# Performance work log

Hardware: AMD Instinct MI355X
Metric: run time of the kernel (lower is better)

The kernel has to match this reference:

```python
import jax, jax.numpy as jnp
import numpy as np

L = 3
NUM_NODES = 4000
NUM_RELS = 200
V = 20
EMB = 128
HID = 128
OUT = 100
N = 50000
E = 800000
B = 32
DECAY = 0.03


def setup_inputs() -> dict:
    key = jax.random.key(0)
    ks = jax.random.split(key, 20)
    s = 0.05  # weight scale
    inp = {
        'node_emb': jax.random.normal(ks[0], (NUM_NODES, EMB), jnp.float32) * s,
        'rel_emb': jax.random.normal(ks[1], (NUM_RELS, EMB), jnp.float32) * s,
        'lin_w': jax.random.normal(ks[2], (HID, EMB), jnp.float32) * s,  # torch Linear weight [out,in]
        'lin_b': jnp.zeros((HID,), jnp.float32),
        'alpha_w': jax.random.normal(ks[3], (L, NUM_NODES, NUM_NODES), jnp.float32) * 0.01,
        'alpha_b': jnp.zeros((L, NUM_NODES), jnp.float32),
        'beta_w': jax.random.normal(ks[4], (L, NUM_NODES), jnp.float32) * 0.01,
        'beta_b': jnp.zeros((L,), jnp.float32),
        'wr_w': jax.random.normal(ks[5], (L, HID), jnp.float32) * s,
        'wr_b': jnp.zeros((L,), jnp.float32),
        'conv_w': jax.random.normal(ks[6], (L, HID, HID), jnp.float32) * s,
        'conv_b': jnp.zeros((L, HID), jnp.float32),
        'mlp_w': jax.random.normal(ks[7], (OUT, 2 * HID), jnp.float32) * s,
        'mlp_b': jnp.zeros((OUT,), jnp.float32),
        'visit_node': jax.random.uniform(ks[8], (B, V, NUM_NODES), jnp.float32),
        'ehr_nodes': jax.random.uniform(ks[9], (B, NUM_NODES), jnp.float32),
        'node_ids': jax.random.randint(ks[10], (N,), 0, NUM_NODES, jnp.int32),
        'rel_ids': jax.random.randint(ks[11], (E,), 0, NUM_RELS, jnp.int32),
        'edge_index': jax.random.randint(ks[12], (2, E), 0, N, jnp.int32),
        'batch': jnp.sort(jax.random.randint(ks[13], (N,), 0, B, jnp.int32)),
    }
    return inp


def reference(node_emb, rel_emb, lin_w, lin_b, alpha_w, alpha_b, beta_w, beta_b,
              wr_w, wr_b, conv_w, conv_b, mlp_w, mlp_b, visit_node, ehr_nodes,
              node_ids, rel_ids, edge_index, batch):
    # initial node / edge features
    x = node_emb[node_ids] @ lin_w.T + lin_b                # [N, HID]
    edge_attr = rel_emb[rel_ids] @ lin_w.T + lin_b          # [E, HID]

    # temporal decay per visit: lambda_j = exp(decay*(V - j)), shape [1, V, 1]
    j = jnp.arange(V, dtype=jnp.float32)
    lam = jnp.exp(DECAY * (V - j))[None, :, None]

    src = edge_index[0]
    dst = edge_index[1]
    xj_nid = node_ids[src]                                  # [E]
    xj_bat = batch[src]                                     # [E]

    for l in range(L):
        # alpha: softmax over the visit axis (dim=1)
        alpha = jax.nn.softmax(
            jnp.einsum('bvn,mn->bvm', visit_node, alpha_w[l]) + alpha_b[l], axis=1)
        beta = jnp.tanh(
            jnp.einsum('bvn,n->bv', visit_node, beta_w[l])[:, :, None] + beta_b[l]) * lam
        attn = jnp.sum(alpha * beta, axis=1)                # [B, NUM_NODES]
        e_attn = attn[xj_bat, xj_nid][:, None]              # [E, 1]

        # BiAttentionGNNConv message + add-aggregate
        w_rel = edge_attr @ wr_w[l][:, None] + wr_b[l]      # [E, 1]
        msg = jax.nn.relu(x[src] * e_attn + w_rel * edge_attr)
        agg = jax.ops.segment_sum(msg, dst, num_segments=N)
        out = agg + x                                       # eps = 0 -> (1+eps)=1
        x = out @ conv_w[l].T + conv_b[l]                   # conv.nn Linear
        x = jax.nn.relu(x)                                  # outer F.relu (dropout inactive in eval)

    # global mean pool over graphs
    cnt = jax.ops.segment_sum(jnp.ones((N,), x.dtype), batch, num_segments=B)
    x_graph = jax.ops.segment_sum(x, batch, num_segments=B) / jnp.maximum(cnt, 1.0)[:, None]

    # patient node embedding branch
    x_node = (ehr_nodes @ node_emb) / jnp.sum(ehr_nodes, axis=1, keepdims=True)
    x_node = x_node @ lin_w.T + lin_b                       # [B, HID]

    logits = jnp.concatenate([x_graph, x_node], axis=1) @ mlp_w.T + mlp_b
    return logits
```

## Files before the change

kernel.cpp:

```cpp
#include <hip/hip_runtime.h>
#include <hip/hip_bf16.h>
#include <stdint.h>

#define LL      3
#define NNODES  4000
#define NRELS   200
#define VV      20
#define EMB     128
#define HIDD    128
#define OUTD    100
#define WS_N    50000
#define WS_E    800000
#define BV      32
#define DECAYF  0.03f
#define AK      4032
#define ZSTRIDE ((long)LL*640*4000)
#define SCAN_NB 196
#define NPP     391
#define CVT_NB  (BV*VV + LL*NNODES)
#define CNT_NB  ((WS_E+255)/256)

typedef __bf16 bf16x8 __attribute__((ext_vector_type(8)));
typedef __bf16 bf16x4 __attribute__((ext_vector_type(4)));
typedef __bf16 bf16x2 __attribute__((ext_vector_type(2)));
typedef float  f32x4  __attribute__((ext_vector_type(4)));

__device__ __forceinline__ void glds16(const __bf16* g, __bf16* l) {
    __builtin_amdgcn_global_load_lds((const __attribute__((address_space(1))) void*)g,
                                     (__attribute__((address_space(3))) void*)l, 16, 0, 0);
}

__global__ __launch_bounds__(256) void k_cvt2(const float* __restrict__ visit,
                                              const float* __restrict__ alpha_w,
                                              const float* __restrict__ beta_w,
                                              const float* __restrict__ beta_b,
                                              __bf16* __restrict__ visit_bf,
                                              __bf16* __restrict__ alpha_bf,
                                              float* __restrict__ betab,
                                              const int* __restrict__ edst,
                                              int* __restrict__ deg) {
    long bid = blockIdx.x;
    int t = threadIdx.x;
    if (bid >= CVT_NB) {
        int e = (int)(bid - CVT_NB)*256 + t;
        if (e < WS_E) atomicAdd(&deg[edst[e]], 1);
        return;
    }
    const bool isv = bid < BV*VV;
    const float* ip; __bf16* op;
    if (isv) { ip = visit + bid*4000; op = visit_bf + bid*AK; }
    else     { long r = bid - BV*VV; ip = alpha_w + r*4000; op = alpha_bf + r*AK; }
    float p0 = 0.f, p1 = 0.f, p2 = 0.f;
    if (t < 250) {
        const float4* p4 = (const float4*)ip + t*4;
        float4 f0 = p4[0], f1 = p4[1], f2 = p4[2], f3 = p4[3];
        bf16x8 h0, h1;
        h0[0]=(__bf16)f0.x; h0[1]=(__bf16)f0.y; h0[2]=(__bf16)f0.z; h0[3]=(__bf16)f0.w;
        h0[4]=(__bf16)f1.x; h0[5]=(__bf16)f1.y; h0[6]=(__bf16)f1.z; h0[7]=(__bf16)f1.w;
        h1[0]=(__bf16)f2.x; h1[1]=(__bf16)f2.y; h1[2]=(__bf16)f2.z; h1[3]=(__bf16)f2.w;
        h1[4]=(__bf16)f3.x; h1[5]=(__bf16)f3.y; h1[6]=(__bf16)f3.z; h1[7]=(__bf16)f3.w;
        ((bf16x8*)op)[t*2]   = h0;
        ((bf16x8*)op)[t*2+1] = h1;
        if (isv) {
            #pragma unroll
            for (int l = 0; l < LL; l++) {
                const float4* bw = (const float4*)(beta_w + (long)l*4000) + t*4;
                float4 b0 = bw[0], b1 = bw[1], b2 = bw[2], b3 = bw[3];
                float s = f0.x*b0.x + f0.y*b0.y + f0.z*b0.z + f0.w*b0.w
                        + f1.x*b1.x + f1.y*b1.y + f1.z*b1.z + f1.w*b1.w
                        + f2.x*b2.x + f2.y*b2.y + f2.z*b2.z + f2.w*b2.w
                        + f3.x*b3.x + f3.y*b3.y + f3.z*b3.z + f3.w*b3.w;
                if (l == 0) p0 = s; else if (l == 1) p1 = s; else p2 = s;
            }
        }
    } else if (t < 254) {
        bf16x8 zz;
        #pragma unroll
        for (int j = 0; j < 8; j++) zz[j] = (__bf16)0.f;
        ((bf16x8*)op)[500 + (t - 250)] = zz;
    }
    if (isv) {
        __shared__ float r0[256], r1[256], r2[256];
        r0[t] = p0; r1[t] = p1; r2[t] = p2;
        __syncthreads();
        for (int o = 128; o > 0; o >>= 1) {
            if (t < o) { r0[t] += r0[t+o]; r1[t] += r1[t+o]; r2[t] += r2[t+o]; }
            __syncthreads();
        }
        if (t == 0) {
            int v = (int)(bid % VV);
            float lam = __expf(DECAYF * (float)(VV - v));
            betab[0*BV*VV + bid] = tanhf(r0[0] + beta_b[0]) * lam;
            betab[1*BV*VV + bid] = tanhf(r1[0] + beta_b[1]) * lam;
            betab[2*BV*VV + bid] = tanhf(r2[0] + beta_b[2]) * lam;
        }
    }
}

__global__ __launch_bounds__(256)
void gemm_alpha(const __bf16* __restrict__ visit_bf, const __bf16* __restrict__ alpha_bf,
                __bf16* __restrict__ zpart)
{
    __shared__ __bf16 Ah[128*64];
    __shared__ __bf16 Bh[128*64];

    const int id   = blockIdx.x;
    const int xcd  = id & 7;
    const int slot = id >> 3;
    const int mi   = slot % 5;
    const int gix  = slot / 5;
    const int g    = xcd * 48 + gix;
    const int ni   = g & 31;
    const int lkh  = g >> 5;
    const int l    = lkh >> 2;
    const int kh   = lkh & 3;

    const __bf16* Ag = visit_bf;
    const __bf16* Bg = alpha_bf + (long)l * NNODES * AK;
    __bf16*       Cg = zpart + (long)kh * ZSTRIDE + (long)l * 640 * 4000;
    const int m0 = mi * 128;
    const int n0 = ni * 128;
    const int k0 = kh * 1024;
    const int k1 = (kh == 3) ? AK : (k0 + 1024);

    const int tid = threadIdx.x;
    const int wv  = tid >> 6;
    const int ln  = tid & 63;
    const int srow = ln >> 3;
    const int gsl  = (ln & 7) ^ srow;

    const __bf16* aA = Ag + (long)(m0 + wv*8 + srow) * AK + gsl*8;
    const __bf16* bB[4];
    #pragma unroll
    for (int t = 0; t < 4; t++) {
        int br = n0 + wv*8 + srow + t*32;
        if (br > NNODES-1) br = NNODES-1;
        bB[t] = Bg + (long)br * AK + gsl*8;
    }

    const int wm = (wv & 1) * 64;
    const int wn = (wv >> 1) * 64;
    const int lr = ln & 15;
    const int kq = ln >> 4;
    const int sw0 = lr & 7;

    f32x4 acc[4][4];
    #pragma unroll
    for (int i = 0; i < 4; i++)
        #pragma unroll
        for (int j = 0; j < 4; j++)
            acc[i][j] = (f32x4){0.f, 0.f, 0.f, 0.f};

    for (int kb = k0; kb < k1; kb += 64) {
        #pragma unroll
        for (int t = 0; t < 4; t++) {
            glds16(aA + (long)t*32*AK + kb, &Ah[(t*4 + wv) * 512]);
            glds16(bB[t] + kb,              &Bh[(t*4 + wv) * 512]);
        }
        __syncthreads();
        #pragma unroll
        for (int ks = 0; ks < 2; ks++) {
            const int sg = ((ks*4 + kq) ^ sw0) * 8;
            bf16x8 af[4], bfr[4];
            #pragma unroll
            for (int i = 0; i < 4; i++) {
                af[i]  = *(const bf16x8*)&Ah[(wm + i*16 + lr)*64 + sg];
                bfr[i] = *(const bf16x8*)&Bh[(wn + i*16 + lr)*64 + sg];
            }
            #pragma unroll
            for (int i = 0; i < 4; i++)
                #pragma unroll
                for (int j = 0; j < 4; j++)
                    acc[i][j] = __builtin_amdgcn_mfma_f32_16x16x32_bf16(af[i], bfr[j], acc[i][j], 0, 0, 0);
        }
        __syncthreads();
    }

    #pragma unroll
    for (int i = 0; i < 4; i++) {
        const int row_b = m0 + wm + i*16 + kq*4;
        #pragma unroll
        for (int j = 0; j < 4; j++) {
            const int col = n0 + wn + j*16 + lr;
            if (col < NNODES) {
                #pragma unroll
                for (int r = 0; r < 4; r++)
                    Cg[(long)(row_b + r)*4000 + col] = (__bf16)acc[i][j][r];
            }
        }
    }
}

#define BM 128
#define BN 128
#define BKG 32
#define LSTR 40

template<int SPLIT>
__device__ __forceinline__ void stage_tile(const float* __restrict__ G, int rows, int Kdim,
                                           int r0, int kb, int k1, __bf16* Sh, __bf16* Sl, int tid)
{
    const int sr  = tid >> 1;
    const int skc = (tid & 1) * 16;
    const int gr  = r0 + sr;
    const int gk  = kb + skc;
    float va[16];
    if (gr < rows && gk + 16 <= k1) {
        const float4* p4 = (const float4*)(G + (long)gr * Kdim + gk);
        #pragma unroll
        for (int q = 0; q < 4; q++) {
            float4 f = p4[q];
            va[4*q+0] = f.x; va[4*q+1] = f.y; va[4*q+2] = f.z; va[4*q+3] = f.w;
        }
    } else {
        #pragma unroll
        for (int j = 0; j < 16; j++) {
            int kk = gk + j;
            va[j] = (gr < rows && kk < k1) ? G[(long)gr * Kdim + kk] : 0.0f;
        }
    }
    bf16x8 h[2], lo[2];
    #pragma unroll
    for (int half = 0; half < 2; half++) {
        #pragma unroll
        for (int j = 0; j < 8; j++) {
            float v = va[half*8 + j];
            __bf16 hi = (__bf16)v;
            h[half][j]  = hi;
            lo[half][j] = (__bf16)(v - (float)hi);
        }
    }
    *(bf16x8*)&Sh[sr*LSTR + skc]     = h[0];
    *(bf16x8*)&Sh[sr*LSTR + skc + 8] = h[1];
    if (SPLIT) {
        *(bf16x8*)&Sl[sr*LSTR + skc]     = lo[0];
        *(bf16x8*)&Sl[sr*LSTR + skc + 8] = lo[1];
    }
}

template<int SPLIT, int RELU, int BIAS, int WRITEB>
__global__ __launch_bounds__(256)
void gemm_bt(const float* __restrict__ Ag, const float* __restrict__ Bg,
             float* __restrict__ Cg, const float* __restrict__ bias,
             __bf16* __restrict__ Xb, int M, int N, int K)
{
    __shared__ __bf16 Ah[BM*LSTR];
    __shared__ __bf16 Bh[BN*LSTR];
    __shared__ __bf16 Alo[SPLIT ? BM*LSTR : 1];
    __shared__ __bf16 Blo[SPLIT ? BN*LSTR : 1];

    const int tid = threadIdx.x;
    const int m0 = blockIdx.x * BM;
    const int n0 = blockIdx.y * BN;

    const int wave = tid >> 6;
    const int lane = tid & 63;
    const int wm = (wave & 1) * 64;
    const int wn = (wave >> 1) * 64;
    const int lr = lane & 15;
    const int kq = lane >> 4;

    f32x4 acc[4][4];
    #pragma unroll
    for (int i = 0; i < 4; i++)
        #pragma unroll
        for (int j = 0; j < 4; j++)
            acc[i][j] = (f32x4){0.f, 0.f, 0.f, 0.f};

    for (int kb = 0; kb < K; kb += BKG) {
        stage_tile<SPLIT>(Ag, M, K, m0, kb, K, Ah, Alo, tid);
        stage_tile<SPLIT>(Bg, N, K, n0, kb, K, Bh, Blo, tid);
        __syncthreads();

        bf16x8 af[4], bfr[4];
        #pragma unroll
        for (int i = 0; i < 4; i++) {
            af[i]  = *(const bf16x8*)&Ah[(wm + i*16 + lr)*LSTR + kq*8];
            bfr[i] = *(const bf16x8*)&Bh[(wn + i*16 + lr)*LSTR + kq*8];
        }
        #pragma unroll
        for (int i = 0; i < 4; i++)
            #pragma unroll
            for (int j = 0; j < 4; j++)
                acc[i][j] = __builtin_amdgcn_mfma_f32_16x16x32_bf16(af[i], bfr[j], acc[i][j], 0, 0, 0);

        if (SPLIT) {
            bf16x8 al[4], bl[4];
            #pragma unroll
            for (int i = 0; i < 4; i++) {
                al[i] = *(const bf16x8*)&Alo[(wm + i*16 + lr)*LSTR + kq*8];
                bl[i] = *(const bf16x8*)&Blo[(wn + i*16 + lr)*LSTR + kq*8];
            }
            #pragma unroll
            for (int i = 0; i < 4; i++)
                #pragma unroll
                for (int j = 0; j < 4; j++) {
                    acc[i][j] = __builtin_amdgcn_mfma_f32_16x16x32_bf16(af[i], bl[j], acc[i][j], 0, 0, 0);
                    acc[i][j] = __builtin_amdgcn_mfma_f32_16x16x32_bf16(al[i], bfr[j], acc[i][j], 0, 0, 0);
                }
        }
        __syncthreads();
    }

    #pragma unroll
    for (int i = 0; i < 4; i++) {
        const int row_b = m0 + wm + i*16 + kq*4;
        #pragma unroll
        for (int j = 0; j < 4; j++) {
            const int col = n0 + wn + j*16 + lr;
            if (col < N) {
                #pragma unroll
                for (int r = 0; r < 4; r++) {
                    const int row = row_b + r;
                    if (row < M) {
                        float v = acc[i][j][r];
                        if (BIAS) v += bias[col];
                        if (RELU) v = fmaxf(v, 0.0f);
                        Cg[(long)row*N + col] = v;
                        if (WRITEB) Xb[(long)row*N + col] = (__bf16)v;
                    }
                }
            }
        }
    }
}

__global__ __launch_bounds__(256) void k_scan1(const int* __restrict__ deg, int* __restrict__ bsum) {
    __shared__ int red[256];
    int t = threadIdx.x;
    int i = blockIdx.x*256 + t;
    red[t] = (i < WS_N) ? deg[i] : 0;
    __syncthreads();
    for (int o = 128; o > 0; o >>= 1) {
        if (t < o) red[t] += red[t + o];
        __syncthreads();
    }
    if (t == 0) bsum[blockIdx.x] = red[0];
}

__global__ __launch_bounds__(256) void k_scan3(const int* __restrict__ deg, const int* __restrict__ bsum,
                                               int* __restrict__ offs, int* __restrict__ cursor) {
    __shared__ int sb[256];
    __shared__ int s[256];
    int t = threadIdx.x;
    int bv = (t < SCAN_NB) ? bsum[t] : 0;
    sb[t] = bv;
    __syncthreads();
    for (int o = 1; o < 256; o <<= 1) {
        int add = (t >= o) ? sb[t - o] : 0;
        __syncthreads();
        sb[t] += add;
        __syncthreads();
    }
    int base = (blockIdx.x == 0) ? 0 : sb[blockIdx.x - 1];

    int i = blockIdx.x*256 + t;
    int v = (i < WS_N) ? deg[i] : 0;
    s[t] = v;
    __syncthreads();
    for (int o = 1; o < 256; o <<= 1) {
        int add = (t >= o) ? s[t - o] : 0;
        __syncthreads();
        s[t] += add;
        __syncthreads();
    }
    if (i < WS_N) {
        int e = base + s[t] - v;
        offs[i] = e;
        cursor[i] = e;
    }
    if (blockIdx.x == 0 && t == 0) offs[WS_N] = WS_E;
}

__global__ void k_fill(const int* __restrict__ dst, const int* __restrict__ src,
                       const int* __restrict__ rel, int* __restrict__ cursor,
                       uint32_t* __restrict__ sr) {
    int e = blockIdx.x*256 + threadIdx.x;
    if (e < WS_E) {
        int d = dst[e];
        int p = atomicAdd(&cursor[d], 1);
        sr[p] = (uint32_t)src[e] | ((uint32_t)rel[e] << 16);
    }
}

__global__ __launch_bounds__(128) void k_relfused(const float* __restrict__ rel_emb,
                                                  const float* __restrict__ lin_w,
                                                  const float* __restrict__ lin_b,
                                                  const float* __restrict__ wr_w,
                                                  const float* __restrict__ wr_b,
                                                  __bf16* __restrict__ relmsg) {
    int r = blockIdx.x;
    int o = threadIdx.x;
    __shared__ float row[128];
    __shared__ float red[128];
    row[o] = rel_emb[(long)r*EMB + o];
    __syncthreads();
    float wv = lin_b[o];
    #pragma unroll 4
    for (int k = 0; k < EMB; k++) wv += row[k] * lin_w[(long)o*EMB + k];
    #pragma unroll
    for (int l = 0; l < LL; l++) {
        red[o] = wv * wr_w[l*HIDD + o];
        __syncthreads();
        for (int s2 = 64; s2 > 0; s2 >>= 1) {
            if (o < s2) red[o] += red[o + s2];
            __syncthreads();
        }
        float wrel = red[0] + wr_b[l];
        __syncthreads();
        relmsg[((long)l*NRELS + r)*HIDD + o] = (__bf16)(wrel * wv);
    }
}

__global__ void k_xinit(const float* __restrict__ Wnode, const int* __restrict__ nid,
                        const int* __restrict__ batch, const float* __restrict__ attn,
                        float* __restrict__ x, __bf16* __restrict__ xb, float* __restrict__ an) {
    int t = blockIdx.x*256 + threadIdx.x;
    if (t >= WS_N*32) return;
    int i = t >> 5;
    int d = t & 31;
    int n = nid[i];
    float4 v = ((const float4*)Wnode)[n*32 + d];
    ((float4*)x)[i*32 + d] = v;
    bf16x4 b;
    b[0] = (__bf16)v.x; b[1] = (__bf16)v.y; b[2] = (__bf16)v.z; b[3] = (__bf16)v.w;
    ((bf16x4*)xb)[i*32 + d] = b;
    if (d < LL) an[(long)d*WS_N + i] = attn[((long)d*BV + batch[i]) * NNODES + n];
}

__global__ __launch_bounds__(256) void k_attnpool(const __bf16* __restrict__ zpart,
                                                  const float* __restrict__ beta, float* __restrict__ attn) {
    int m = blockIdx.x*256 + threadIdx.x;
    int b = blockIdx.y;
    int l = blockIdx.z;
    if (m >= NNODES) return;
    const __bf16* zp = zpart + ((long)l*640 + b*VV) * 4000 + m;
    const float* bet = beta + (l*BV + b) * VV;
    float zv[VV];
    float mx = -1e30f;
    #pragma unroll
    for (int v = 0; v < VV; v++) {
        long o = (long)v * 4000;
        float s = (float)zp[o] + (float)zp[ZSTRIDE + o] + (float)zp[2*ZSTRIDE + o] + (float)zp[3*ZSTRIDE + o];
        zv[v] = s;
        mx = fmaxf(mx, s);
    }
    float s = 0.f, ws = 0.f;
    #pragma unroll
    for (int v = 0; v < VV; v++) {
        float e = __expf(zv[v] - mx);
        s += e;
        ws += e * bet[v];
    }
    attn[((long)l*BV + b) * NNODES + m] = ws / s;
}

__global__ __launch_bounds__(256) void k_agg(const float* __restrict__ x, const __bf16* __restrict__ xb,
                                             const float* __restrict__ an,
                                             const __bf16* __restrict__ relmsg_l, const int* __restrict__ offs,
                                             const uint32_t* __restrict__ sr,
                                             float* __restrict__ outb) {
    int node = blockIdx.x*4 + (threadIdx.x >> 6);
    int lane = threadIdx.x & 63;
    int eh = lane >> 4;
    int lh = lane & 15;
    int e0 = offs[node], e1 = offs[node + 1];
    const bf16x8* xb8 = (const bf16x8*)xb;
    const bf16x8* rm8 = (const bf16x8*)relmsg_l;
    float acc[8];
    #pragma unroll
    for (int d = 0; d < 8; d++) acc[d] = 0.f;
    int e = e0;
    for (; e + 8 <= e1; e += 8) {
        uint32_t p0 = sr[e + eh], p1 = sr[e + 4 + eh];
        int s0 = p0 & 0xFFFF, r0 = p0 >> 16;
        int s1 = p1 & 0xFFFF, r1 = p1 >> 16;
        float a0 = an[s0], a1 = an[s1];
        bf16x8 g0 = xb8[s0*16 + lh], g1 = xb8[s1*16 + lh];
        bf16x8 m0 = rm8[r0*16 + lh], m1 = rm8[r1*16 + lh];
        #pragma unroll
        for (int d = 0; d < 8; d++) {
            acc[d] += fmaxf((float)g0[d]*a0 + (float)m0[d], 0.f);
            acc[d] += fmaxf((float)g1[d]*a1 + (float)m1[d], 0.f);
        }
    }
    for (; e + 4 <= e1; e += 4) {
        uint32_t p = sr[e + eh];
        int s = p & 0xFFFF, r = p >> 16;
        float a = an[s];
        bf16x8 g = xb8[s*16 + lh];
        bf16x8 m = rm8[r*16 + lh];
        #pragma unroll
        for (int d = 0; d < 8; d++)
            acc[d] += fmaxf((float)g[d]*a + (float)m[d], 0.f);
    }
    if (e + eh < e1) {
        uint32_t p = sr[e + eh];
        int s = p & 0xFFFF, r = p >> 16;
        float a = an[s];
        bf16x8 g = xb8[s*16 + lh];
        bf16x8 m = rm8[r*16 + lh];
        #pragma unroll
        for (int d = 0; d < 8; d++)
            acc[d] += fmaxf((float)g[d]*a + (float)m[d], 0.f);
    }
    #pragma unroll
    for (int d = 0; d < 8; d++) {
        acc[d] += __shfl_xor(acc[d], 16);
        acc[d] += __shfl_xor(acc[d], 32);
    }
    if (eh == 0) {
        float4 x0 = ((const float4*)x)[node*32 + lh*2];
        float4 x1 = ((const float4*)x)[node*32 + lh*2 + 1];
        float4 o0, o1;
        o0.x = acc[0] + x0.x; o0.y = acc[1] + x0.y; o0.z = acc[2] + x0.z; o0.w = acc[3] + x0.w;
        o1.x = acc[4] + x1.x; o1.y = acc[5] + x1.y; o1.z = acc[6] + x1.z; o1.w = acc[7] + x1.w;
        ((float4*)outb)[node*32 + lh*2]     = o0;
        ((float4*)outb)[node*32 + lh*2 + 1] = o1;
    }
}

__global__ __launch_bounds__(256) void k_pool(const float* __restrict__ x,
                                              const int* __restrict__ batch,
                                              const float* __restrict__ ehr,
                                              const float* __restrict__ node_emb,
                                              float* __restrict__ xgsum,
                                              float* __restrict__ xnsum,
                                              float* __restrict__ esum) {
    if (blockIdx.x < NPP) {
        int r0 = blockIdx.x * 128;
        int d = threadIdx.x & 127;
        int rofs = threadIdx.x >> 7;
        int r1 = min(r0 + 128, WS_N);
        float acc = 0.f;
        int curb = -1;
        for (int i = r0 + rofs; i < r1; i += 2) {
            int b = batch[i];
            if (b != curb) {
                if (curb >= 0) atomicAdd(&xgsum[curb*HIDD + d], acc);
                acc = 0.f; curb = b;
            }
            acc += x[(long)i*HIDD + d];
        }
        if (curb >= 0) atomicAdd(&xgsum[curb*HIDD + d], acc);
    } else {
        int id = blockIdx.x - NPP;
        int b = id >> 4;
        int c = id & 15;
        int d = threadIdx.x;
        int n0 = c * (NNODES/16), n1 = n0 + (NNODES/16);
        __shared__ float red[256];
        if (d < 128) {
            float acc = 0.f;
            for (int n = n0; n < n1; n++)
                acc += ehr[b*NNODES + n] * node_emb[(long)n*HIDD + d];
            atomicAdd(&xnsum[b*HIDD + d], acc);
        }
        float s = 0.f;
        for (int n = n0 + d; n < n1; n += 256) s += ehr[b*NNODES + n];
        red[d] = s; __syncthreads();
        for (int o = 128; o > 0; o >>= 1) {
            if (d < o) red[d] += red[d + o];
            __syncthreads();
        }
        if (d == 0) atomicAdd(&esum[b], red[0]);
    }
}

__global__ __launch_bounds__(128) void k_head(const float* __restrict__ xgsum,
                                              const float* __restrict__ xnsum,
                                              const float* __restrict__ esum,
                                              const int* __restrict__ batch,
                                              const float* __restrict__ lin_w, const float* __restrict__ lin_b,
                                              const float* __restrict__ mlp_w, const float* __restrict__ mlp_b,
                                              float* __restrict__ out) {
    int b = blockIdx.x;
    int d = threadIdx.x;
    int lo = 0, hi = WS_N;
    while (lo < hi) { int mid = (lo + hi) >> 1; if (batch[mid] < b) lo = mid + 1; else hi = mid; }
    int s0 = lo;
    lo = 0; hi = WS_N;
    while (lo < hi) { int mid = (lo + hi) >> 1; if (batch[mid] < b + 1) lo = mid + 1; else hi = mid; }
    int cnt = max(lo - s0, 1);
    __shared__ float t1[128];
    __shared__ float cat[2*HIDD];
    t1[d]  = xnsum[b*HIDD + d] / esum[b];
    cat[d] = xgsum[b*HIDD + d] / (float)cnt;
    __syncthreads();
    float o2 = lin_b[d];
    for (int k2 = 0; k2 < HIDD; k2++) o2 += t1[k2] * lin_w[d*HIDD + k2];
    cat[HIDD + d] = o2;
    __syncthreads();
    if (d < OUTD) {
        float a = mlp_b[d];
        for (int j = 0; j < 2*HIDD; j++) a += cat[j] * mlp_w[d*2*HIDD + j];
        out[b*OUTD + d] = a;
    }
}

extern "C" void kernel_launch(void* const* d_in, const int* in_sizes, int n_in,
                              void* d_out, int out_size, void* d_ws, size_t ws_size,
                              hipStream_t stream)
{
    const float* node_emb = (const float*)d_in[0];
    const float* rel_emb  = (const float*)d_in[1];
    const float* lin_w    = (const float*)d_in[2];
    const float* lin_b    = (const float*)d_in[3];
    const float* alpha_w  = (const float*)d_in[4];
    const float* beta_w   = (const float*)d_in[6];
    const float* beta_b   = (const float*)d_in[7];
    const float* wr_w     = (const float*)d_in[8];
    const float* wr_b     = (const float*)d_in[9];
    const float* conv_w   = (const float*)d_in[10];
    const float* conv_b   = (const float*)d_in[11];
    const float* mlp_w    = (const float*)d_in[12];
    const float* mlp_b    = (const float*)d_in[13];
    const float* visit    = (const float*)d_in[14];
    const float* ehr      = (const float*)d_in[15];
    const int* node_ids   = (const int*)d_in[16];
    const int* rel_ids    = (const int*)d_in[17];
    const int* ei         = (const int*)d_in[18];
    const int* batch      = (const int*)d_in[19];
    const int* esrc = ei;
    const int* edst = ei + WS_E;
    float* out = (float*)d_out;

    char* p = (char*)d_ws;
    auto take = [&](size_t bytes) -> char* {
        char* q = p;
        p += (bytes + 255) & ~(size_t)255;
        return q;
    };
    __bf16* zpart    = (__bf16*)take((size_t)4*ZSTRIDE*2);
    __bf16* visit_bf = (__bf16*)take((size_t)(BV*VV)*AK*2);
    char*   big      = take((size_t)LL*NNODES*AK*2);
    float* betab  = (float*)take((size_t)LL*BV*VV*4);
    float* xgsum  = (float*)take((size_t)BV*HIDD*4);
    float* xnsum  = (float*)take((size_t)BV*HIDD*4);
    float* esum   = (float*)take((size_t)BV*4);
    int* deg      = (int*)take((size_t)WS_N*4);
    size_t zero_bytes = (size_t)((char*)(deg + WS_N) - (char*)xgsum);
    int* offs     = (int*)take((size_t)(WS_N+1)*4);
    int* cursor   = (int*)take((size_t)WS_N*4);
    int* bsum     = (int*)take((size_t)SCAN_NB*4);
    if ((size_t)(p - (char*)d_ws) > ws_size) return;

    __bf16* alpha_bf = (__bf16*)big;
    char* q = big;
    auto carve = [&](size_t bytes) -> char* {
        char* r = q;
        q += (bytes + 255) & ~(size_t)255;
        return r;
    };
    float*    x      = (float*)carve((size_t)WS_N*HIDD*4);
    __bf16*   xb     = (__bf16*)carve((size_t)WS_N*HIDD*2);
    uint32_t* sr     = (uint32_t*)carve((size_t)WS_E*4);
    float*    attn   = (float*)carve((size_t)LL*BV*NNODES*4);
    float*    attnnd = (float*)carve((size_t)LL*WS_N*4);
    float*    Wnode  = (float*)carve((size_t)NNODES*HIDD*4);
    __bf16*   relmsg = (__bf16*)carve((size_t)LL*NRELS*HIDD*2);
    float*    aggbuf = (float*)zpart;

    (void)hipMemsetAsync(xgsum, 0, zero_bytes, stream);

    k_cvt2<<<dim3(CVT_NB + CNT_NB), 256, 0, stream>>>(visit, alpha_w, beta_w, beta_b,
                                                      visit_bf, alpha_bf, betab, edst, deg);
    gemm_alpha<<<dim3(1920), 256, 0, stream>>>(visit_bf, alpha_bf, zpart);
    k_attnpool<<<dim3((NNODES+255)/256, BV, LL), 256, 0, stream>>>(zpart, betab, attn);

    k_scan1<<<dim3(SCAN_NB), 256, 0, stream>>>(deg, bsum);
    k_scan3<<<dim3(SCAN_NB), 256, 0, stream>>>(deg, bsum, offs, cursor);
    k_fill<<<dim3((WS_E+255)/256), 256, 0, stream>>>(edst, esrc, rel_ids, cursor, sr);

    gemm_bt<1,0,1,0><<<dim3((NNODES+BM-1)/BM, 1, 1), 256, 0, stream>>>(
        node_emb, lin_w, Wnode, lin_b, nullptr, NNODES, HIDD, HIDD);
    k_relfused<<<dim3(NRELS), 128, 0, stream>>>(rel_emb, lin_w, lin_b, wr_w, wr_b, relmsg);
    k_xinit<<<dim3((WS_N*32+255)/256), 256, 0, stream>>>(Wnode, node_ids, batch, attn, x, xb, attnnd);

    for (int l = 0; l < LL; l++) {
        k_agg<<<dim3(WS_N/4), 256, 0, stream>>>(
            x, xb, attnnd + (size_t)l*WS_N, relmsg + (size_t)l*NRELS*HIDD, offs, sr, aggbuf);
        if (l < LL-1)
            gemm_bt<1,1,1,1><<<dim3((WS_N+BM-1)/BM, 1, 1), 256, 0, stream>>>(
                aggbuf, conv_w + (size_t)l*HIDD*HIDD, x, conv_b + (size_t)l*HIDD, xb,
                WS_N, HIDD, HIDD);
        else
            gemm_bt<1,1,1,0><<<dim3((WS_N+BM-1)/BM, 1, 1), 256, 0, stream>>>(
                aggbuf, conv_w + (size_t)l*HIDD*HIDD, x, conv_b + (size_t)l*HIDD, nullptr,
                WS_N, HIDD, HIDD);
    }

    k_pool<<<dim3(NPP + 16*BV), 256, 0, stream>>>(x, batch, ehr, node_emb, xgsum, xnsum, esum);
    k_head<<<BV, 128, 0, stream>>>(xgsum, xnsum, esum, batch, lin_w, lin_b, mlp_w, mlp_b, out);
}
```

Measured before the change: 771.5 us.

## Use nontemporal memory ops, rebalance conversion blocks, move degree count into GEMM

The alpha-weight conversion now handles two rows per block, and the visit and alpha paths are split so visit blocks always do the beta reduction. The edge-degree atomic counting moves from the conversion kernel into extra blocks of the alpha GEMM launch. Nontemporal loads and stores are added for streaming data (conversion, GEMM outputs, z partials, x pooling, the aggregation A operand). The aggregation loop also software-prefetches the next packed edge indices. The aim is to cut cache pollution and launch-tail costs, at the risk of losing L2 reuse where data is re-read soon after.

```diff
diff --git a/kernel.cpp b/kernel.cpp
--- a/kernel.cpp
+++ b/kernel.cpp
@@ -17,17 +17,30 @@
 #define ZSTRIDE ((long)LL*640*4000)
 #define SCAN_NB 196
 #define NPP     391
-#define CVT_NB  (BV*VV + LL*NNODES)
 #define CNT_NB  ((WS_E+255)/256)
+#define GA_NB   1920
+#define CVA_NB  ((LL*NNODES)/2)
 
 typedef __bf16 bf16x8 __attribute__((ext_vector_type(8)));
 typedef __bf16 bf16x4 __attribute__((ext_vector_type(4)));
 typedef __bf16 bf16x2 __attribute__((ext_vector_type(2)));
 typedef float  f32x4  __attribute__((ext_vector_type(4)));
+typedef unsigned short u16x8 __attribute__((ext_vector_type(8)));
 
 __device__ __forceinline__ void glds16(const __bf16* g, __bf16* l) {
     __builtin_amdgcn_global_load_lds((const __attribute__((address_space(1))) void*)g,
                                      (__attribute__((address_space(3))) void*)l, 16, 0, 0);
+}
+
+__device__ __forceinline__ u16x8 pack8(f32x4 f0, f32x4 f1) {
+    bf16x8 h;
+    h[0]=(__bf16)f0.x; h[1]=(__bf16)f0.y; h[2]=(__bf16)f0.z; h[3]=(__bf16)f0.w;
+    h[4]=(__bf16)f1.x; h[5]=(__bf16)f1.y; h[6]=(__bf16)f1.z; h[7]=(__bf16)f1.w;
+    return __builtin_bit_cast(u16x8, h);
+}
+
+__device__ __forceinline__ float bfu_to_f32(unsigned short u) {
+    return __builtin_bit_cast(float, ((unsigned)u) << 16);
 }
 
 __global__ __launch_bounds__(256) void k_cvt2(const float* __restrict__ visit,
@@ -36,75 +49,92 @@
                                               const float* __restrict__ beta_b,
                                               __bf16* __restrict__ visit_bf,
                                               __bf16* __restrict__ alpha_bf,
-                                              float* __restrict__ betab,
-                                              const int* __restrict__ edst,
-                                              int* __restrict__ deg) {
-    long bid = blockIdx.x;
+                                              float* __restrict__ betab) {
+    int bid = blockIdx.x;
     int t = threadIdx.x;
-    if (bid >= CVT_NB) {
-        int e = (int)(bid - CVT_NB)*256 + t;
-        if (e < WS_E) atomicAdd(&deg[edst[e]], 1);
+    if (bid >= BV*VV) {
+        long r0 = (long)(bid - BV*VV) * 2;
+        const f32x4* pa = (const f32x4*)alpha_w + r0*1000;
+        const f32x4* pb = pa + 1000;
+        __bf16* oa = alpha_bf + r0*AK;
+        __bf16* ob = oa + AK;
+        if (t < 250) {
+            const f32x4* qa = pa + t*4;
+            const f32x4* qb = pb + t*4;
+            f32x4 a0 = __builtin_nontemporal_load(qa);
+            f32x4 a1 = __builtin_nontemporal_load(qa+1);
+            f32x4 a2 = __builtin_nontemporal_load(qa+2);
+            f32x4 a3 = __builtin_nontemporal_load(qa+3);
+            f32x4 b0 = __builtin_nontemporal_load(qb);
+            f32x4 b1 = __builtin_nontemporal_load(qb+1);
+            f32x4 b2 = __builtin_nontemporal_load(qb+2);
+            f32x4 b3 = __builtin_nontemporal_load(qb+3);
+            __builtin_nontemporal_store(pack8(a0,a1), (u16x8*)oa + t*2);
+            __builtin_nontemporal_store(pack8(a2,a3), (u16x8*)oa + t*2 + 1);
+            __builtin_nontemporal_store(pack8(b0,b1), (u16x8*)ob + t*2);
+            __builtin_nontemporal_store(pack8(b2,b3), (u16x8*)ob + t*2 + 1);
+        } else if (t < 254) {
+            u16x8 zz = (u16x8)0;
+            ((u16x8*)oa)[500 + (t - 250)] = zz;
+            ((u16x8*)ob)[500 + (t - 250)] = zz;
+        }
         return;
     }
-    const bool isv = bid < BV*VV;
-    const float* ip; __bf16* op;
-    if (isv) { ip = visit + bid*4000; op = visit_bf + bid*AK; }
-    else     { long r = bid - BV*VV; ip = alpha_w + r*4000; op = alpha_bf + r*AK; }
+    const float* ip = visit + (long)bid*4000;
+    __bf16* op = visit_bf + (long)bid*AK;
     float p0 = 0.f, p1 = 0.f, p2 = 0.f;
     if (t < 250) {
-        const float4* p4 = (const float4*)ip + t*4;
-        float4 f0 = p4[0], f1 = p4[1], f2 = p4[2], f3 = p4[3];
-        bf16x8 h0, h1;
-        h0[0]=(__bf16)f0.x; h0[1]=(__bf16)f0.y; h0[2]=(__bf16)f0.z; h0[3]=(__bf16)f0.w;
-        h0[4]=(__bf16)f1.x; h0[5]=(__bf16)f1.y; h0[6]=(__bf16)f1.z; h0[7]=(__bf16)f1.w;
-        h1[0]=(__bf16)f2.x; h1[1]=(__bf16)f2.y; h1[2]=(__bf16)f2.z; h1[3]=(__bf16)f2.w;
-        h1[4]=(__bf16)f3.x; h1[5]=(__bf16)f3.y; h1[6]=(__bf16)f3.z; h1[7]=(__bf16)f3.w;
-        ((bf16x8*)op)[t*2]   = h0;
-        ((bf16x8*)op)[t*2+1] = h1;
-        if (isv) {
-            #pragma unroll
-            for (int l = 0; l < LL; l++) {
-                const float4* bw = (const float4*)(beta_w + (long)l*4000) + t*4;
-                float4 b0 = bw[0], b1 = bw[1], b2 = bw[2], b3 = bw[3];
-                float s = f0.x*b0.x + f0.y*b0.y + f0.z*b0.z + f0.w*b0.w
-                        + f1.x*b1.x + f1.y*b1.y + f1.z*b1.z + f1.w*b1.w
-                        + f2.x*b2.x + f2.y*b2.y + f2.z*b2.z + f2.w*b2.w
-                        + f3.x*b3.x + f3.y*b3.y + f3.z*b3.z + f3.w*b3.w;
-                if (l == 0) p0 = s; else if (l == 1) p1 = s; else p2 = s;
-            }
+        const f32x4* p4 = (const f32x4*)ip + t*4;
+        f32x4 f0 = __builtin_nontemporal_load(p4);
+        f32x4 f1 = __builtin_nontemporal_load(p4+1);
+        f32x4 f2 = __builtin_nontemporal_load(p4+2);
+        f32x4 f3 = __builtin_nontemporal_load(p4+3);
+        __builtin_nontemporal_store(pack8(f0,f1), (u16x8*)op + t*2);
+        __builtin_nontemporal_store(pack8(f2,f3), (u16x8*)op + t*2 + 1);
+        #pragma unroll
+        for (int l = 0; l < LL; l++) {
+            const f32x4* bw = (const f32x4*)(beta_w + (long)l*4000) + t*4;
+            f32x4 b0 = bw[0], b1 = bw[1], b2 = bw[2], b3 = bw[3];
+            float s = f0.x*b0.x + f0.y*b0.y + f0.z*b0.z + f0.w*b0.w
+                    + f1.x*b1.x + f1.y*b1.y + f1.z*b1.z + f1.w*b1.w
+                    + f2.x*b2.x + f2.y*b2.y + f2.z*b2.z + f2.w*b2.w
+                    + f3.x*b3.x + f3.y*b3.y + f3.z*b3.z + f3.w*b3.w;
+            if (l == 0) p0 = s; else if (l == 1) p1 = s; else p2 = s;
         }
     } else if (t < 254) {
-        bf16x8 zz;
-        #pragma unroll
-        for (int j = 0; j < 8; j++) zz[j] = (__bf16)0.f;
-        ((bf16x8*)op)[500 + (t - 250)] = zz;
-    }
-    if (isv) {
-        __shared__ float r0[256], r1[256], r2[256];
-        r0[t] = p0; r1[t] = p1; r2[t] = p2;
-        __syncthreads();
-        for (int o = 128; o > 0; o >>= 1) {
-            if (t < o) { r0[t] += r0[t+o]; r1[t] += r1[t+o]; r2[t] += r2[t+o]; }
-            __syncthreads();
-        }
-        if (t == 0) {
-            int v = (int)(bid % VV);
-            float lam = __expf(DECAYF * (float)(VV - v));
-            betab[0*BV*VV + bid] = tanhf(r0[0] + beta_b[0]) * lam;
-            betab[1*BV*VV + bid] = tanhf(r1[0] + beta_b[1]) * lam;
-            betab[2*BV*VV + bid] = tanhf(r2[0] + beta_b[2]) * lam;
-        }
+        u16x8 zz = (u16x8)0;
+        ((u16x8*)op)[500 + (t - 250)] = zz;
+    }
+    __shared__ float r0s[256], r1s[256], r2s[256];
+    r0s[t] = p0; r1s[t] = p1; r2s[t] = p2;
+    __syncthreads();
+    for (int o = 128; o > 0; o >>= 1) {
+        if (t < o) { r0s[t] += r0s[t+o]; r1s[t] += r1s[t+o]; r2s[t] += r2s[t+o]; }
+        __syncthreads();
+    }
+    if (t == 0) {
+        int v = bid % VV;
+        float lam = __expf(DECAYF * (float)(VV - v));
+        betab[0*BV*VV + bid] = tanhf(r0s[0] + beta_b[0]) * lam;
+        betab[1*BV*VV + bid] = tanhf(r1s[0] + beta_b[1]) * lam;
+        betab[2*BV*VV + bid] = tanhf(r2s[0] + beta_b[2]) * lam;
     }
 }
 
 __global__ __launch_bounds__(256)
 void gemm_alpha(const __bf16* __restrict__ visit_bf, const __bf16* __restrict__ alpha_bf,
-                __bf16* __restrict__ zpart)
+                __bf16* __restrict__ zpart,
+                const int* __restrict__ edst, int* __restrict__ deg)
 {
     __shared__ __bf16 Ah[128*64];
     __shared__ __bf16 Bh[128*64];
 
     const int id   = blockIdx.x;
+    if (id >= GA_NB) {
+        int e = (id - GA_NB)*256 + threadIdx.x;
+        if (e < WS_E) atomicAdd(&deg[edst[e]], 1);
+        return;
+    }
     const int xcd  = id & 7;
     const int slot = id >> 3;
     const int mi   = slot % 5;
@@ -184,8 +214,10 @@
             const int col = n0 + wn + j*16 + lr;
             if (col < NNODES) {
                 #pragma unroll
-                for (int r = 0; r < 4; r++)
-                    Cg[(long)(row_b + r)*4000 + col] = (__bf16)acc[i][j][r];
+                for (int r = 0; r < 4; r++) {
+                    unsigned short cv = __builtin_bit_cast(unsigned short, (__bf16)acc[i][j][r]);
+                    __builtin_nontemporal_store(cv, (unsigned short*)&Cg[(long)(row_b + r)*4000 + col]);
+                }
             }
         }
     }
@@ -196,7 +228,7 @@
 #define BKG 32
 #define LSTR 40
 
-template<int SPLIT>
+template<int SPLIT, int NT>
 __device__ __forceinline__ void stage_tile(const float* __restrict__ G, int rows, int Kdim,
                                            int r0, int kb, int k1, __bf16* Sh, __bf16* Sl, int tid)
 {
@@ -206,10 +238,10 @@
     const int gk  = kb + skc;
     float va[16];
     if (gr < rows && gk + 16 <= k1) {
-        const float4* p4 = (const float4*)(G + (long)gr * Kdim + gk);
+        const f32x4* p4 = (const f32x4*)(G + (long)gr * Kdim + gk);
         #pragma unroll
         for (int q = 0; q < 4; q++) {
-            float4 f = p4[q];
+            f32x4 f = NT ? __builtin_nontemporal_load(p4 + q) : p4[q];
             va[4*q+0] = f.x; va[4*q+1] = f.y; va[4*q+2] = f.z; va[4*q+3] = f.w;
         }
     } else {
@@ -268,8 +300,8 @@
             acc[i][j] = (f32x4){0.f, 0.f, 0.f, 0.f};
 
     for (int kb = 0; kb < K; kb += BKG) {
-        stage_tile<SPLIT>(Ag, M, K, m0, kb, K, Ah, Alo, tid);
-        stage_tile<SPLIT>(Bg, N, K, n0, kb, K, Bh, Blo, tid);
+        stage_tile<SPLIT,1>(Ag, M, K, m0, kb, K, Ah, Alo, tid);
+        stage_tile<SPLIT,0>(Bg, N, K, n0, kb, K, Bh, Blo, tid);
         __syncthreads();
 
         bf16x8 af[4], bfr[4];
@@ -434,14 +466,17 @@
     int b = blockIdx.y;
     int l = blockIdx.z;
     if (m >= NNODES) return;
-    const __bf16* zp = zpart + ((long)l*640 + b*VV) * 4000 + m;
+    const unsigned short* zp = (const unsigned short*)zpart + ((long)l*640 + b*VV) * 4000 + m;
     const float* bet = beta + (l*BV + b) * VV;
     float zv[VV];
     float mx = -1e30f;
     #pragma unroll
     for (int v = 0; v < VV; v++) {
         long o = (long)v * 4000;
-        float s = (float)zp[o] + (float)zp[ZSTRIDE + o] + (float)zp[2*ZSTRIDE + o] + (float)zp[3*ZSTRIDE + o];
+        float s = bfu_to_f32(__builtin_nontemporal_load(&zp[o]))
+                + bfu_to_f32(__builtin_nontemporal_load(&zp[ZSTRIDE + o]))
+                + bfu_to_f32(__builtin_nontemporal_load(&zp[2*ZSTRIDE + o]))
+                + bfu_to_f32(__builtin_nontemporal_load(&zp[3*ZSTRIDE + o]));
         zv[v] = s;
         mx = fmaxf(mx, s);
     }
@@ -471,10 +506,16 @@
     #pragma unroll
     for (int d = 0; d < 8; d++) acc[d] = 0.f;
     int e = e0;
-    for (; e + 8 <= e1; e += 8) {
-        uint32_t p0 = sr[e + eh], p1 = sr[e + 4 + eh];
-        int s0 = p0 & 0xFFFF, r0 = p0 >> 16;
-        int s1 = p1 & 0xFFFF, r1 = p1 >> 16;
+    uint32_t p0 = 0, p1 = 0;
+    bool have = (e + 8 <= e1);
+    if (have) { p0 = sr[e + eh]; p1 = sr[e + 4 + eh]; }
+    while (have) {
+        uint32_t c0 = p0, c1 = p1;
+        int en = e + 8;
+        bool haven = (en + 8 <= e1);
+        if (haven) { p0 = sr[en + eh]; p1 = sr[en + 4 + eh]; }
+        int s0 = c0 & 0xFFFF, r0 = c0 >> 16;
+        int s1 = c1 & 0xFFFF, r1 = c1 >> 16;
         float a0 = an[s0], a1 = an[s1];
         bf16x8 g0 = xb8[s0*16 + lh], g1 = xb8[s1*16 + lh];
         bf16x8 m0 = rm8[r0*16 + lh], m1 = rm8[r1*16 + lh];
@@ -483,6 +524,7 @@
             acc[d] += fmaxf((float)g0[d]*a0 + (float)m0[d], 0.f);
             acc[d] += fmaxf((float)g1[d]*a1 + (float)m1[d], 0.f);
         }
+        e = en; have = haven;
     }
     for (; e + 4 <= e1; e += 4) {
         uint32_t p = sr[e + eh];
@@ -540,7 +582,7 @@
                 if (curb >= 0) atomicAdd(&xgsum[curb*HIDD + d], acc);
                 acc = 0.f; curb = b;
             }
-            acc += x[(long)i*HIDD + d];
+            acc += __builtin_nontemporal_load(&x[(long)i*HIDD + d]);
         }
         if (curb >= 0) atomicAdd(&xgsum[curb*HIDD + d], acc);
     } else {
@@ -663,9 +705,9 @@
 
     (void)hipMemsetAsync(xgsum, 0, zero_bytes, stream);
 
-    k_cvt2<<<dim3(CVT_NB + CNT_NB), 256, 0, stream>>>(visit, alpha_w, beta_w, beta_b,
-                                                      visit_bf, alpha_bf, betab, edst, deg);
-    gemm_alpha<<<dim3(1920), 256, 0, stream>>>(visit_bf, alpha_bf, zpart);
+    k_cvt2<<<dim3(BV*VV + CVA_NB), 256, 0, stream>>>(visit, alpha_w, beta_w, beta_b,
+                                                     visit_bf, alpha_bf, betab);
+    gemm_alpha<<<dim3(GA_NB + CNT_NB), 256, 0, stream>>>(visit_bf, alpha_bf, zpart, edst, deg);
     k_attnpool<<<dim3((NNODES+255)/256, BV, LL), 256, 0, stream>>>(zpart, betab, attn);
 
     k_scan1<<<dim3(SCAN_NB), 256, 0, stream>>>(deg, bsum);
```

New measurement: 801.0 us. 3.8% more time.
